# Performance work log

Hardware: AMD Instinct MI355X
Metric: run time of the kernel (lower is better)

Reference implementation:

```python
import jax, jax.numpy as jnp
import numpy as np


def _eta(pos, conj):
    # e[0] = pos[:,1::2] repeated into even/odd cols; e[1] = (+/-)pos[:,0::2] likewise
    c = jnp.repeat(pos[:, 1::2], 2, axis=1)
    s = jnp.repeat(pos[:, 0::2], 2, axis=1)
    return jnp.stack([c, s if conj else -s])  # [2, N, d]


def setup_inputs() -> dict:
    key = jax.random.key(0)
    ks = jax.random.split(key, 8)
    B, N, d, H = 8, 4096, 128, 4
    s = 0.02
    return {
        "x": jax.random.normal(ks[0], (B, N, d), jnp.float32),
        "pos": jax.random.normal(ks[1], (N, d), jnp.float32),
        "W_lt": jax.random.normal(ks[2], (d, d), jnp.float32) * s,
        "W_phi": jax.random.normal(ks[3], (d * H, d), jnp.float32) * s,
        "b_phi": jnp.zeros((d * H,), jnp.float32),
        "W_c1": jax.random.normal(ks[4], (H, H), jnp.float32) * s,
        "b_c1": jnp.zeros((H,), jnp.float32),
        "W_c2": jax.random.normal(ks[5], (1, H), jnp.float32) * s,
        "b_c2": jnp.zeros((1,), jnp.float32),
        "ln_g": jnp.ones((d,), jnp.float32),
        "ln_b": jnp.zeros((d,), jnp.float32),
        "W_f1": jax.random.normal(ks[6], (d, d), jnp.float32) * s,
        "b_f1": jnp.zeros((d,), jnp.float32),
        "W_f2": jax.random.normal(ks[7], (d, d), jnp.float32) * s,
        "b_f2": jnp.zeros((d,), jnp.float32),
    }


def reference(x, pos, W_lt, W_phi, b_phi, W_c1, b_c1, W_c2, b_c2,
              ln_g, ln_b, W_f1, b_f1, W_f2, b_f2):
    B, N, d = x.shape
    H = W_phi.shape[0] // d
    x = x @ W_lt.T                                   # linear_trans (no bias)
    e = _eta(pos, False)                             # [2,N,d]
    xe = x[None] * e[:, None]                        # [2,B,N,d]
    # A = ones(N,N) - I  =>  A @ v == sum over nodes minus self
    f = xe.sum(axis=2, keepdims=True) - xe           # [2,B,N,d]
    f_norm = jnp.sqrt(f[0] ** 2 + f[1] ** 2)         # [B,N,d]
    phi = ((x + pos[None]) @ W_phi.T + b_phi).reshape(B, N, H, d)
    # ReLU1(|f| - phi): relu(min(1, f_norm - phi))
    res = jax.nn.relu(jnp.minimum(1.0, f_norm[:, :, None, :] - phi))  # [B,N,H,d]
    ce = _eta(pos, True)
    fec = f[0] * ce[0][None] - f[1] * ce[1][None]    # [B,N,d]
    rfe = res * fec[:, :, None, :]                   # [B,N,H,d]
    # inverse transform: (1/N) * (M @ A) with A symmetric => sum-minus-self over node dim
    inv = (rfe.sum(axis=1, keepdims=True) - rfe) / N  # [B,N,H,d]
    t = inv.transpose(0, 1, 3, 2)                    # [B,N,d,H]
    comb = (jax.nn.relu(t @ W_c1.T + b_c1) @ W_c2.T + b_c2)[..., 0]  # [B,N,d]
    m = x + comb
    mu = m.mean(-1, keepdims=True)
    var = ((m - mu) ** 2).mean(-1, keepdims=True)
    mn = (m - mu) * jax.lax.rsqrt(var + 1e-6) * ln_g + ln_b
    return jax.nn.relu(mn @ W_f1.T + b_f1) @ W_f2.T + b_f2
```

## Files before the change

### kernel.cpp

```cpp
#include <hip/hip_runtime.h>
#include <hip/hip_bf16.h>


#define DEV __device__ __forceinline__

typedef __attribute__((ext_vector_type(8))) short bf16x8;
typedef __attribute__((ext_vector_type(4))) float f32x4;

constexpr int Bb = 8, Nn = 4096;
constexpr int BN = Bb * Nn;
constexpr int LDP = 136;
constexpr int P8  = 144;

union U8 { ushort u[8]; uint4 v; };

static DEV ushort f2bf(float f) {
    __hip_bfloat16 h = __float2bfloat16(f);
    return *reinterpret_cast<unsigned short*>(&h);
}
static DEV float bf2f(ushort u) {
    return __bfloat162float(*reinterpret_cast<const __hip_bfloat16*>(&u));
}
static DEV unsigned char f2fp8(float f) {
    return (unsigned char)(__builtin_amdgcn_cvt_pk_fp8_f32(f, f, 0u, false) & 0xff);
}

__global__ __launch_bounds__(256) void k_fused1(
    const float* __restrict__ X, const float* __restrict__ Wlt,
    const float* __restrict__ Wphi, const float* __restrict__ bphi,
    const float* __restrict__ pos, ushort* __restrict__ x1b,
    unsigned char* __restrict__ phi8, float* __restrict__ PS)
{
    __shared__ __align__(16) ushort xs[64 * LDP];
    __shared__ __align__(16) ushort wsl[128 * LDP];
    __shared__ __align__(16) unsigned char aux[64 * P8];
    float (*red)[2][128] = reinterpret_cast<float (*)[2][128]>(aux);
    unsigned char* p8 = aux;

    const int t = threadIdx.x;
    const int row0 = blockIdx.x * 64;
    const int w = t >> 6, l = t & 63;
    const int lr = l & 15;
    const int lk = (l >> 4) * 8;

    #pragma unroll
    for (int i = 0; i < 4; ++i) {
        int e = t + i * 256, r = e >> 4, c = (e & 15) * 8;
        const float* p = X + (size_t)(row0 + r) * 128 + c;
        float4 a = *reinterpret_cast<const float4*>(p);
        float4 b = *reinterpret_cast<const float4*>(p + 4);
        U8 u;
        u.u[0] = f2bf(a.x); u.u[1] = f2bf(a.y); u.u[2] = f2bf(a.z); u.u[3] = f2bf(a.w);
        u.u[4] = f2bf(b.x); u.u[5] = f2bf(b.y); u.u[6] = f2bf(b.z); u.u[7] = f2bf(b.w);
        *reinterpret_cast<uint4*>(xs + r * LDP + c) = u.v;
    }
    #pragma unroll
    for (int i = 0; i < 8; ++i) {
        int e = t + i * 256, r = e >> 4, c = (e & 15) * 8;
        const float* p = Wlt + (size_t)r * 128 + c;
        float4 a = *reinterpret_cast<const float4*>(p);
        float4 b = *reinterpret_cast<const float4*>(p + 4);
        U8 u;
        u.u[0] = f2bf(a.x); u.u[1] = f2bf(a.y); u.u[2] = f2bf(a.z); u.u[3] = f2bf(a.w);
        u.u[4] = f2bf(b.x); u.u[5] = f2bf(b.y); u.u[6] = f2bf(b.z); u.u[7] = f2bf(b.w);
        *reinterpret_cast<uint4*>(wsl + r * LDP + c) = u.v;
    }
    __syncthreads();

    {
        f32x4 acc[8];
        #pragma unroll
        for (int cf = 0; cf < 8; ++cf) acc[cf] = f32x4{0.f, 0.f, 0.f, 0.f};
        #pragma unroll
        for (int ks = 0; ks < 4; ++ks) {
            bf16x8 a = *reinterpret_cast<const bf16x8*>(xs + (w * 16 + lr) * LDP + ks * 32 + lk);
            #pragma unroll
            for (int cf = 0; cf < 8; ++cf) {
                bf16x8 b = *reinterpret_cast<const bf16x8*>(wsl + (cf * 16 + lr) * LDP + ks * 32 + lk);
                acc[cf] = __builtin_amdgcn_mfma_f32_16x16x32_bf16(a, b, acc[cf], 0, 0, 0);
            }
        }
        __syncthreads();

        #pragma unroll
        for (int cf = 0; cf < 8; ++cf) {
            int col = cf * 16 + lr;
            #pragma unroll
            for (int reg = 0; reg < 4; ++reg) {
                int rl = w * 16 + (l >> 4) * 4 + reg;
                xs[rl * LDP + col] = f2bf(acc[cf][reg]);
            }
        }
    }
    __syncthreads();

    #pragma unroll
    for (int i = 0; i < 4; ++i) {
        int e = t + i * 256, r = e >> 4, c = (e & 15) * 8;
        uint4 v = *reinterpret_cast<const uint4*>(xs + r * LDP + c);
        *reinterpret_cast<uint4*>(x1b + (size_t)(row0 + r) * 128 + c) = v;
    }
    {
        int c2 = t & 63, g = t >> 6;
        float a0e = 0.f, a1e = 0.f, a0o = 0.f, a1o = 0.f;
        #pragma unroll 4
        for (int i = 0; i < 16; ++i) {
            int r = g * 16 + i;
            int n = (row0 + r) & (Nn - 1);
            unsigned int v = *reinterpret_cast<const unsigned int*>(xs + r * LDP + 2 * c2);
            float lo = bf2f((ushort)(v & 0xffff));
            float hi = bf2f((ushort)(v >> 16));
            float2 p = *reinterpret_cast<const float2*>(pos + (size_t)n * 128 + 2 * c2);
            a0e += lo * p.y; a1e += lo * p.x;
            a0o += hi * p.y; a1o += hi * p.x;
        }
        red[g][0][2 * c2] = a0e; red[g][0][2 * c2 + 1] = a0o;
        red[g][1][2 * c2] = a1e; red[g][1][2 * c2 + 1] = a1o;
    }
    __syncthreads();

    {
        int half = t >> 7, col = t & 127;
        float s = red[0][half][col] + red[1][half][col] + red[2][half][col] + red[3][half][col];
        PS[(size_t)blockIdx.x * 256 + t] = s;
    }
    #pragma unroll
    for (int i = 0; i < 4; ++i) {
        int e = t + i * 256, r = e >> 4, c = (e & 15) * 8;
        U8 u;
        u.v = *reinterpret_cast<const uint4*>(xs + r * LDP + c);
        int n = (row0 + r) & (Nn - 1);
        const float* q = pos + (size_t)n * 128 + c;
        float4 pa = *reinterpret_cast<const float4*>(q);
        float4 pb = *reinterpret_cast<const float4*>(q + 4);
        u.u[0] = f2bf(bf2f(u.u[0]) + pa.x);
        u.u[1] = f2bf(bf2f(u.u[1]) + pa.y);
        u.u[2] = f2bf(bf2f(u.u[2]) + pa.z);
        u.u[3] = f2bf(bf2f(u.u[3]) + pa.w);
        u.u[4] = f2bf(bf2f(u.u[4]) + pb.x);
        u.u[5] = f2bf(bf2f(u.u[5]) + pb.y);
        u.u[6] = f2bf(bf2f(u.u[6]) + pb.z);
        u.u[7] = f2bf(bf2f(u.u[7]) + pb.w);
        *reinterpret_cast<uint4*>(xs + r * LDP + c) = u.v;
    }

    for (int jt = 0; jt < 4; ++jt) {
        __syncthreads();
        {
            const float* Wt = Wphi + (size_t)jt * 128 * 128;
            #pragma unroll
            for (int i = 0; i < 8; ++i) {
                int e = t + i * 256, r = e >> 4, c = (e & 15) * 8;
                const float* p = Wt + (size_t)r * 128 + c;
                float4 a = *reinterpret_cast<const float4*>(p);
                float4 b = *reinterpret_cast<const float4*>(p + 4);
                U8 u;
                u.u[0] = f2bf(a.x); u.u[1] = f2bf(a.y); u.u[2] = f2bf(a.z); u.u[3] = f2bf(a.w);
                u.u[4] = f2bf(b.x); u.u[5] = f2bf(b.y); u.u[6] = f2bf(b.z); u.u[7] = f2bf(b.w);
                *reinterpret_cast<uint4*>(wsl + r * LDP + c) = u.v;
            }
            if (jt > 0) {
                #pragma unroll
                for (int i = 0; i < 2; ++i) {
                    int e = t + i * 256, r = e >> 3, c = (e & 7) * 16;
                    uint4 v = *reinterpret_cast<const uint4*>(p8 + r * P8 + c);
                    *reinterpret_cast<uint4*>(phi8 + (size_t)(row0 + r) * 512 + (jt - 1) * 128 + c) = v;
                }
            }
        }
        __syncthreads();

        f32x4 acc[8];
        #pragma unroll
        for (int cf = 0; cf < 8; ++cf) acc[cf] = f32x4{0.f, 0.f, 0.f, 0.f};
        #pragma unroll
        for (int ks = 0; ks < 4; ++ks) {
            bf16x8 a = *reinterpret_cast<const bf16x8*>(xs + (w * 16 + lr) * LDP + ks * 32 + lk);
            #pragma unroll
            for (int cf = 0; cf < 8; ++cf) {
                bf16x8 b = *reinterpret_cast<const bf16x8*>(wsl + (cf * 16 + lr) * LDP + ks * 32 + lk);
                acc[cf] = __builtin_amdgcn_mfma_f32_16x16x32_bf16(a, b, acc[cf], 0, 0, 0);
            }
        }
        #pragma unroll
        for (int cf = 0; cf < 8; ++cf) {
            int col = cf * 16 + lr;
            float bv = bphi[jt * 128 + col];
            #pragma unroll
            for (int reg = 0; reg < 4; ++reg) {
                int rl = w * 16 + (l >> 4) * 4 + reg;
                p8[rl * P8 + col] = f2fp8(acc[cf][reg] + bv);
            }
        }
    }
    __syncthreads();
    #pragma unroll
    for (int i = 0; i < 2; ++i) {
        int e = t + i * 256, r = e >> 3, c = (e & 7) * 16;
        uint4 v = *reinterpret_cast<const uint4*>(p8 + r * P8 + c);
        *reinterpret_cast<uint4*>(phi8 + (size_t)(row0 + r) * 512 + 3 * 128 + c) = v;
    }
}

__global__ __launch_bounds__(256) void k_finS(
    const float* __restrict__ PS, float* __restrict__ S0, float* __restrict__ S1)
{
    int b = blockIdx.x, t = threadIdx.x;
    float s = 0.f;
    #pragma unroll 8
    for (int c = 0; c < 64; ++c) s += PS[(size_t)(b * 64 + c) * 256 + t];
    if (t < 128) S0[b * 128 + t] = s;
    else         S1[b * 128 + (t - 128)] = s;
}

__global__ __launch_bounds__(256) void k_reduceT(
    const ushort* __restrict__ x1b, const unsigned char* __restrict__ phi8,
    const float* __restrict__ pos, const float* __restrict__ S0,
    const float* __restrict__ S1, float* __restrict__ PT)
{
    int b = blockIdx.x >> 6, c64 = blockIdx.x & 63;
    int rr = threadIdx.x >> 5, d0 = (threadIdx.x & 31) * 4;
    float4 S0v = *reinterpret_cast<const float4*>(S0 + b * 128 + d0);
    float4 S1v = *reinterpret_cast<const float4*>(S1 + b * 128 + d0);
    float S0a[4] = {S0v.x, S0v.y, S0v.z, S0v.w};
    float S1a[4] = {S1v.x, S1v.y, S1v.z, S1v.w};
    float acc[4][4];
    #pragma unroll
    for (int h = 0; h < 4; ++h)
        #pragma unroll
        for (int j = 0; j < 4; ++j) acc[h][j] = 0.f;

    #pragma unroll 2
    for (int i = 0; i < 8; ++i) {
        int n = c64 * 64 + i * 8 + rr;
        size_t r = (size_t)b * Nn + n;
        ushort4 xv4 = *reinterpret_cast<const ushort4*>(x1b + r * 128 + d0);
        float4 p = *reinterpret_cast<const float4*>(pos + (size_t)n * 128 + d0);
        float xv[4] = {bf2f(xv4.x), bf2f(xv4.y), bf2f(xv4.z), bf2f(xv4.w)};
        float cc[4] = {p.y, p.y, p.w, p.w};
        float ss[4] = {p.x, p.x, p.z, p.z};
        float fec[4], fn[4];
        #pragma unroll
        for (int j = 0; j < 4; ++j) {
            float f0 = S0a[j] - xv[j] * cc[j];
            float f1 = xv[j] * ss[j] - S1a[j];
            fn[j] = sqrtf(f0 * f0 + f1 * f1);
            fec[j] = f0 * cc[j] - f1 * ss[j];
        }
        #pragma unroll
        for (int h = 0; h < 4; ++h) {
            unsigned int pv = *reinterpret_cast<const unsigned int*>(phi8 + r * 512 + h * 128 + d0);
            float ph0 = __builtin_amdgcn_cvt_f32_fp8(pv, 0);
            float ph1 = __builtin_amdgcn_cvt_f32_fp8(pv, 1);
            float ph2 = __builtin_amdgcn_cvt_f32_fp8(pv, 2);
            float ph3 = __builtin_amdgcn_cvt_f32_fp8(pv, 3);
            acc[h][0] += fmaxf(0.f, fminf(1.f, fn[0] - ph0)) * fec[0];
            acc[h][1] += fmaxf(0.f, fminf(1.f, fn[1] - ph1)) * fec[1];
            acc[h][2] += fmaxf(0.f, fminf(1.f, fn[2] - ph2)) * fec[2];
            acc[h][3] += fmaxf(0.f, fminf(1.f, fn[3] - ph3)) * fec[3];
        }
    }
    __shared__ float red[8][512];
    #pragma unroll
    for (int h = 0; h < 4; ++h)
        #pragma unroll
        for (int j = 0; j < 4; ++j) red[rr][h * 128 + d0 + j] = acc[h][j];
    __syncthreads();
    int tt = threadIdx.x;
    #pragma unroll
    for (int q = 0; q < 2; ++q) {
        int idx = tt + q * 256;
        float s = 0.f;
        #pragma unroll
        for (int k = 0; k < 8; ++k) s += red[k][idx];
        PT[(size_t)blockIdx.x * 512 + idx] = s;
    }
}

__global__ __launch_bounds__(256) void k_finT(
    const float* __restrict__ PT, float* __restrict__ T)
{
    int idx = blockIdx.x * 256 + threadIdx.x;
    int b = idx >> 9, lo = idx & 511;
    float s = 0.f;
    #pragma unroll 8
    for (int c = 0; c < 64; ++c) s += PT[(size_t)b * 32768 + c * 512 + lo];
    T[idx] = s;
}

__global__ __launch_bounds__(256) void k_comb_ffn(
    const ushort* __restrict__ x1b, const unsigned char* __restrict__ phi8,
    const float* __restrict__ pos, const float* __restrict__ S0,
    const float* __restrict__ S1, const float* __restrict__ T,
    const float* __restrict__ Wc1, const float* __restrict__ bc1,
    const float* __restrict__ Wc2, const float* __restrict__ bc2,
    const float* __restrict__ lng, const float* __restrict__ lnb,
    const float* __restrict__ Wf1, const float* __restrict__ bf1,
    const float* __restrict__ Wf2, const float* __restrict__ bf2,
    float* __restrict__ out)
{
    __shared__ __align__(16) ushort xs[64 * LDP];
    __shared__ __align__(16) ushort wsl[128 * LDP];
    const int t = threadIdx.x;
    const int row0 = blockIdx.x * 64;
    const int w = t >> 6, l = t & 63;

    #pragma unroll
    for (int i = 0; i < 8; ++i) {
        int e = t + i * 256, r = e >> 4, c = (e & 15) * 8;
        const float* p = Wf1 + (size_t)r * 128 + c;
        float4 a = *reinterpret_cast<const float4*>(p);
        float4 b = *reinterpret_cast<const float4*>(p + 4);
        U8 u;
        u.u[0] = f2bf(a.x); u.u[1] = f2bf(a.y); u.u[2] = f2bf(a.z); u.u[3] = f2bf(a.w);
        u.u[4] = f2bf(b.x); u.u[5] = f2bf(b.y); u.u[6] = f2bf(b.z); u.u[7] = f2bf(b.w);
        *reinterpret_cast<uint4*>(wsl + r * LDP + c) = u.v;
    }

    {
        const int d0 = 2 * l;
        const float g0 = lng[d0], g1 = lng[d0 + 1];
        const float be0 = lnb[d0], be1 = lnb[d0 + 1];
        const float c2v[4] = {Wc2[0], Wc2[1], Wc2[2], Wc2[3]};
        const float b2v = bc2[0];
        for (int i = 0; i < 16; ++i) {
            int rl = w * 16 + i;
            int rrow = row0 + rl;
            int b = rrow >> 12;
            int n = rrow & 4095;
            size_t r = (size_t)rrow;

            ushort2 xv2 = *reinterpret_cast<const ushort2*>(x1b + r * 128 + d0);
            float2 p2 = *reinterpret_cast<const float2*>(pos + (size_t)n * 128 + d0);
            float2 s0 = *reinterpret_cast<const float2*>(S0 + b * 128 + d0);
            float2 s1 = *reinterpret_cast<const float2*>(S1 + b * 128 + d0);
            float cc = p2.y, ss = p2.x;
            float xv[2] = {bf2f(xv2.x), bf2f(xv2.y)};
            float S0a[2] = {s0.x, s0.y}, S1a[2] = {s1.x, s1.y};
            float2 Tv[4];
            #pragma unroll
            for (int h = 0; h < 4; ++h)
                Tv[h] = *reinterpret_cast<const float2*>(T + (b * 4 + h) * 128 + d0);
            float phv[4][2];
            #pragma unroll
            for (int h = 0; h < 4; ++h) {
                unsigned int pu = *reinterpret_cast<const ushort*>(phi8 + r * 512 + h * 128 + d0);
                phv[h][0] = __builtin_amdgcn_cvt_f32_fp8(pu, 0);
                phv[h][1] = __builtin_amdgcn_cvt_f32_fp8(pu, 1);
            }

            float m[2];
            #pragma unroll
            for (int q = 0; q < 2; ++q) {
                float f0 = S0a[q] - xv[q] * cc;
                float f1 = xv[q] * ss - S1a[q];
                float fn = sqrtf(f0 * f0 + f1 * f1);
                float fec = f0 * cc - f1 * ss;
                float inv[4];
                #pragma unroll
                for (int h = 0; h < 4; ++h) {
                    float res = fmaxf(0.f, fminf(1.f, fn - phv[h][q]));
                    float tv = q ? Tv[h].y : Tv[h].x;
                    inv[h] = (tv - res * fec) * (1.f / (float)Nn);
                }
                float comb = b2v;
                #pragma unroll
                for (int h = 0; h < 4; ++h) {
                    float u = bc1[h];
                    #pragma unroll
                    for (int h2 = 0; h2 < 4; ++h2) u += Wc1[h * 4 + h2] * inv[h2];
                    comb += fmaxf(u, 0.f) * c2v[h];
                }
                m[q] = xv[q] + comb;
            }

            float s = m[0] + m[1];
            #pragma unroll
            for (int off = 32; off; off >>= 1) s += __shfl_xor(s, off);
            float mu = s * (1.f / 128.f);
            float e0 = m[0] - mu, e1 = m[1] - mu;
            float v = e0 * e0 + e1 * e1;
            #pragma unroll
            for (int off = 32; off; off >>= 1) v += __shfl_xor(v, off);
            float rstd = rsqrtf(v * (1.f / 128.f) + 1e-6f);
            ushort2 o;
            o.x = f2bf(e0 * rstd * g0 + be0);
            o.y = f2bf(e1 * rstd * g1 + be1);
            *reinterpret_cast<ushort2*>(xs + rl * LDP + d0) = o;
        }
    }
    __syncthreads();

    const int lr = l & 15;
    const int lk = (l >> 4) * 8;

    f32x4 acc[8];
    #pragma unroll
    for (int cf = 0; cf < 8; ++cf) acc[cf] = f32x4{0.f, 0.f, 0.f, 0.f};
    #pragma unroll
    for (int ks = 0; ks < 4; ++ks) {
        bf16x8 a = *reinterpret_cast<const bf16x8*>(xs + (w * 16 + lr) * LDP + ks * 32 + lk);
        #pragma unroll
        for (int cf = 0; cf < 8; ++cf) {
            bf16x8 b = *reinterpret_cast<const bf16x8*>(wsl + (cf * 16 + lr) * LDP + ks * 32 + lk);
            acc[cf] = __builtin_amdgcn_mfma_f32_16x16x32_bf16(a, b, acc[cf], 0, 0, 0);
        }
    }
    __syncthreads();

    #pragma unroll
    for (int cf = 0; cf < 8; ++cf) {
        int col = cf * 16 + lr;
        float bv = bf1[col];
        #pragma unroll
        for (int reg = 0; reg < 4; ++reg) {
            int rl = w * 16 + (l >> 4) * 4 + reg;
            xs[rl * LDP + col] = f2bf(fmaxf(acc[cf][reg] + bv, 0.f));
        }
    }
    #pragma unroll
    for (int i = 0; i < 8; ++i) {
        int e = t + i * 256, r = e >> 4, c = (e & 15) * 8;
        const float* p = Wf2 + (size_t)r * 128 + c;
        float4 a = *reinterpret_cast<const float4*>(p);
        float4 b = *reinterpret_cast<const float4*>(p + 4);
        U8 u;
        u.u[0] = f2bf(a.x); u.u[1] = f2bf(a.y); u.u[2] = f2bf(a.z); u.u[3] = f2bf(a.w);
        u.u[4] = f2bf(b.x); u.u[5] = f2bf(b.y); u.u[6] = f2bf(b.z); u.u[7] = f2bf(b.w);
        *reinterpret_cast<uint4*>(wsl + r * LDP + c) = u.v;
    }
    __syncthreads();

    #pragma unroll
    for (int cf = 0; cf < 8; ++cf) acc[cf] = f32x4{0.f, 0.f, 0.f, 0.f};
    #pragma unroll
    for (int ks = 0; ks < 4; ++ks) {
        bf16x8 a = *reinterpret_cast<const bf16x8*>(xs + (w * 16 + lr) * LDP + ks * 32 + lk);
        #pragma unroll
        for (int cf = 0; cf < 8; ++cf) {
            bf16x8 b = *reinterpret_cast<const bf16x8*>(wsl + (cf * 16 + lr) * LDP + ks * 32 + lk);
            acc[cf] = __builtin_amdgcn_mfma_f32_16x16x32_bf16(a, b, acc[cf], 0, 0, 0);
        }
    }
    #pragma unroll
    for (int cf = 0; cf < 8; ++cf) {
        int col = cf * 16 + lr;
        float bv = bf2[col];
        #pragma unroll
        for (int reg = 0; reg < 4; ++reg) {
            int r = row0 + w * 16 + (l >> 4) * 4 + reg;
            out[(size_t)r * 128 + col] = acc[cf][reg] + bv;
        }
    }
}

extern "C" void kernel_launch(void* const* d_in, const int* in_sizes, int n_in,
                              void* d_out, int out_size, void* d_ws, size_t ws_size,
                              hipStream_t stream)
{
    const float* x    = (const float*)d_in[0];
    const float* pos  = (const float*)d_in[1];
    const float* Wlt  = (const float*)d_in[2];
    const float* Wphi = (const float*)d_in[3];
    const float* bphi = (const float*)d_in[4];
    const float* Wc1  = (const float*)d_in[5];
    const float* bc1  = (const float*)d_in[6];
    const float* Wc2  = (const float*)d_in[7];
    const float* bc2  = (const float*)d_in[8];
    const float* lng  = (const float*)d_in[9];
    const float* lnb  = (const float*)d_in[10];
    const float* Wf1  = (const float*)d_in[11];
    const float* bf1  = (const float*)d_in[12];
    const float* Wf2  = (const float*)d_in[13];
    const float* bf2  = (const float*)d_in[14];

    float* ws = (float*)d_ws;
    ushort* x1b = (ushort*)ws;
    float* S0   = ws + 2097152;
    float* S1   = S0 + 1024;
    float* T    = S1 + 1024;
    float* PS   = T + 4096;
    float* PT   = PS + 131072;
    unsigned char* phi8 = (unsigned char*)(ws + 2496512);
    float* out  = (float*)d_out;

    k_fused1<<<dim3(BN / 64), 256, 0, stream>>>(x, Wlt, Wphi, bphi, pos, x1b, phi8, PS);
    k_finS<<<dim3(Bb), 256, 0, stream>>>(PS, S0, S1);
    k_reduceT<<<dim3(512), 256, 0, stream>>>(x1b, phi8, pos, S0, S1, PT);
    k_finT<<<dim3(16), 256, 0, stream>>>(PT, T);
    k_comb_ffn<<<dim3(BN / 64), 256, 0, stream>>>(x1b, phi8, pos, S0, S1, T,
                                                  Wc1, bc1, Wc2, bc2, lng, lnb,
                                                  Wf1, bf1, Wf2, bf2, out);
}
```

Baseline: 70.43 us.

## Pre-convert weights to bf16 once and merge reductions into cooperative kernel

Adds a prep kernel that converts all weight matrices to bf16 in workspace, so the 512 blocks of each GEMM kernel no longer repeat the fp32 load and bf16 conversion. It also replaces the three small reduction kernels (finS, reduceT, finT) with one cooperative kernel that uses grid-wide syncs between phases and warp-shuffle reductions. The aim is to cut launch overhead and redundant conversion work. The cost is one extra launch and a dependency on cooperative launch, which needs all 512 blocks resident at once, plus grid-sync overhead.

```diff
diff --git a/kernel.cpp b/kernel.cpp
--- a/kernel.cpp
+++ b/kernel.cpp
@@ -1,5 +1,8 @@
 #include <hip/hip_runtime.h>
 #include <hip/hip_bf16.h>
+#include <hip/hip_cooperative_groups.h>
+
+namespace cg = cooperative_groups;
 
 
 #define DEV __device__ __forceinline__
@@ -25,9 +28,30 @@
     return (unsigned char)(__builtin_amdgcn_cvt_pk_fp8_f32(f, f, 0u, false) & 0xff);
 }
 
+__global__ __launch_bounds__(256) void k_prep(
+    const float* __restrict__ Wlt, const float* __restrict__ Wphi,
+    const float* __restrict__ Wf1, const float* __restrict__ Wf2,
+    ushort* __restrict__ wbLt, ushort* __restrict__ wbPhi,
+    ushort* __restrict__ wbF1, ushort* __restrict__ wbF2)
+{
+    int bx = blockIdx.x;
+    const float* src; ushort* dst; int off;
+    if (bx < 8)       { src = Wlt;  dst = wbLt;  off = bx * 2048; }
+    else if (bx < 40) { src = Wphi; dst = wbPhi; off = (bx - 8) * 2048; }
+    else if (bx < 48) { src = Wf1;  dst = wbF1;  off = (bx - 40) * 2048; }
+    else              { src = Wf2;  dst = wbF2;  off = (bx - 48) * 2048; }
+    int e = off + threadIdx.x * 8;
+    float4 a = *reinterpret_cast<const float4*>(src + e);
+    float4 b = *reinterpret_cast<const float4*>(src + e + 4);
+    U8 u;
+    u.u[0] = f2bf(a.x); u.u[1] = f2bf(a.y); u.u[2] = f2bf(a.z); u.u[3] = f2bf(a.w);
+    u.u[4] = f2bf(b.x); u.u[5] = f2bf(b.y); u.u[6] = f2bf(b.z); u.u[7] = f2bf(b.w);
+    *reinterpret_cast<uint4*>(dst + e) = u.v;
+}
+
 __global__ __launch_bounds__(256) void k_fused1(
-    const float* __restrict__ X, const float* __restrict__ Wlt,
-    const float* __restrict__ Wphi, const float* __restrict__ bphi,
+    const float* __restrict__ X, const ushort* __restrict__ wbLt,
+    const ushort* __restrict__ wbPhi, const float* __restrict__ bphi,
     const float* __restrict__ pos, ushort* __restrict__ x1b,
     unsigned char* __restrict__ phi8, float* __restrict__ PS)
 {
@@ -57,13 +81,8 @@
     #pragma unroll
     for (int i = 0; i < 8; ++i) {
         int e = t + i * 256, r = e >> 4, c = (e & 15) * 8;
-        const float* p = Wlt + (size_t)r * 128 + c;
-        float4 a = *reinterpret_cast<const float4*>(p);
-        float4 b = *reinterpret_cast<const float4*>(p + 4);
-        U8 u;
-        u.u[0] = f2bf(a.x); u.u[1] = f2bf(a.y); u.u[2] = f2bf(a.z); u.u[3] = f2bf(a.w);
-        u.u[4] = f2bf(b.x); u.u[5] = f2bf(b.y); u.u[6] = f2bf(b.z); u.u[7] = f2bf(b.w);
-        *reinterpret_cast<uint4*>(wsl + r * LDP + c) = u.v;
+        uint4 v = *reinterpret_cast<const uint4*>(wbLt + (size_t)r * 128 + c);
+        *reinterpret_cast<uint4*>(wsl + r * LDP + c) = v;
     }
     __syncthreads();
 
@@ -147,17 +166,12 @@
     for (int jt = 0; jt < 4; ++jt) {
         __syncthreads();
         {
-            const float* Wt = Wphi + (size_t)jt * 128 * 128;
+            const ushort* Wt = wbPhi + (size_t)jt * 128 * 128;
             #pragma unroll
             for (int i = 0; i < 8; ++i) {
                 int e = t + i * 256, r = e >> 4, c = (e & 15) * 8;
-                const float* p = Wt + (size_t)r * 128 + c;
-                float4 a = *reinterpret_cast<const float4*>(p);
-                float4 b = *reinterpret_cast<const float4*>(p + 4);
-                U8 u;
-                u.u[0] = f2bf(a.x); u.u[1] = f2bf(a.y); u.u[2] = f2bf(a.z); u.u[3] = f2bf(a.w);
-                u.u[4] = f2bf(b.x); u.u[5] = f2bf(b.y); u.u[6] = f2bf(b.z); u.u[7] = f2bf(b.w);
-                *reinterpret_cast<uint4*>(wsl + r * LDP + c) = u.v;
+                uint4 v = *reinterpret_cast<const uint4*>(Wt + (size_t)r * 128 + c);
+                *reinterpret_cast<uint4*>(wsl + r * LDP + c) = v;
             }
             if (jt > 0) {
                 #pragma unroll
@@ -202,90 +216,101 @@
     }
 }
 
-__global__ __launch_bounds__(256) void k_finS(
-    const float* __restrict__ PS, float* __restrict__ S0, float* __restrict__ S1)
+__global__ __launch_bounds__(256) void k_coop_ST(
+    const ushort* __restrict__ x1b, const unsigned char* __restrict__ phi8,
+    const float* __restrict__ pos, const float* __restrict__ PS,
+    float* __restrict__ S0, float* __restrict__ S1,
+    float* __restrict__ PT, float* __restrict__ T)
 {
-    int b = blockIdx.x, t = threadIdx.x;
-    float s = 0.f;
-    #pragma unroll 8
-    for (int c = 0; c < 64; ++c) s += PS[(size_t)(b * 64 + c) * 256 + t];
-    if (t < 128) S0[b * 128 + t] = s;
-    else         S1[b * 128 + (t - 128)] = s;
-}
-
-__global__ __launch_bounds__(256) void k_reduceT(
-    const ushort* __restrict__ x1b, const unsigned char* __restrict__ phi8,
-    const float* __restrict__ pos, const float* __restrict__ S0,
-    const float* __restrict__ S1, float* __restrict__ PT)
-{
-    int b = blockIdx.x >> 6, c64 = blockIdx.x & 63;
-    int rr = threadIdx.x >> 5, d0 = (threadIdx.x & 31) * 4;
-    float4 S0v = *reinterpret_cast<const float4*>(S0 + b * 128 + d0);
-    float4 S1v = *reinterpret_cast<const float4*>(S1 + b * 128 + d0);
-    float S0a[4] = {S0v.x, S0v.y, S0v.z, S0v.w};
-    float S1a[4] = {S1v.x, S1v.y, S1v.z, S1v.w};
-    float acc[4][4];
-    #pragma unroll
-    for (int h = 0; h < 4; ++h)
-        #pragma unroll
-        for (int j = 0; j < 4; ++j) acc[h][j] = 0.f;
-
-    #pragma unroll 2
-    for (int i = 0; i < 8; ++i) {
-        int n = c64 * 64 + i * 8 + rr;
-        size_t r = (size_t)b * Nn + n;
-        ushort4 xv4 = *reinterpret_cast<const ushort4*>(x1b + r * 128 + d0);
-        float4 p = *reinterpret_cast<const float4*>(pos + (size_t)n * 128 + d0);
-        float xv[4] = {bf2f(xv4.x), bf2f(xv4.y), bf2f(xv4.z), bf2f(xv4.w)};
-        float cc[4] = {p.y, p.y, p.w, p.w};
-        float ss[4] = {p.x, p.x, p.z, p.z};
-        float fec[4], fn[4];
-        #pragma unroll
-        for (int j = 0; j < 4; ++j) {
-            float f0 = S0a[j] - xv[j] * cc[j];
-            float f1 = xv[j] * ss[j] - S1a[j];
-            fn[j] = sqrtf(f0 * f0 + f1 * f1);
-            fec[j] = f0 * cc[j] - f1 * ss[j];
-        }
-        #pragma unroll
-        for (int h = 0; h < 4; ++h) {
-            unsigned int pv = *reinterpret_cast<const unsigned int*>(phi8 + r * 512 + h * 128 + d0);
-            float ph0 = __builtin_amdgcn_cvt_f32_fp8(pv, 0);
-            float ph1 = __builtin_amdgcn_cvt_f32_fp8(pv, 1);
-            float ph2 = __builtin_amdgcn_cvt_f32_fp8(pv, 2);
-            float ph3 = __builtin_amdgcn_cvt_f32_fp8(pv, 3);
-            acc[h][0] += fmaxf(0.f, fminf(1.f, fn[0] - ph0)) * fec[0];
-            acc[h][1] += fmaxf(0.f, fminf(1.f, fn[1] - ph1)) * fec[1];
-            acc[h][2] += fmaxf(0.f, fminf(1.f, fn[2] - ph2)) * fec[2];
-            acc[h][3] += fmaxf(0.f, fminf(1.f, fn[3] - ph3)) * fec[3];
-        }
-    }
-    __shared__ float red[8][512];
-    #pragma unroll
-    for (int h = 0; h < 4; ++h)
-        #pragma unroll
-        for (int j = 0; j < 4; ++j) red[rr][h * 128 + d0 + j] = acc[h][j];
-    __syncthreads();
-    int tt = threadIdx.x;
-    #pragma unroll
-    for (int q = 0; q < 2; ++q) {
-        int idx = tt + q * 256;
-        float s = 0.f;
-        #pragma unroll
-        for (int k = 0; k < 8; ++k) s += red[k][idx];
-        PT[(size_t)blockIdx.x * 512 + idx] = s;
-    }
-}
-
-__global__ __launch_bounds__(256) void k_finT(
-    const float* __restrict__ PT, float* __restrict__ T)
-{
-    int idx = blockIdx.x * 256 + threadIdx.x;
-    int b = idx >> 9, lo = idx & 511;
-    float s = 0.f;
-    #pragma unroll 8
-    for (int c = 0; c < 64; ++c) s += PT[(size_t)b * 32768 + c * 512 + lo];
-    T[idx] = s;
+    cg::grid_group grid = cg::this_grid();
+
+    {
+        int idx = blockIdx.x * 4 + (threadIdx.x >> 6);
+        int lane = threadIdx.x & 63;
+        int b = idx >> 8, tcol = idx & 255;
+        float s = PS[(size_t)(b * 64 + lane) * 256 + tcol];
+        #pragma unroll
+        for (int off = 32; off; off >>= 1) s += __shfl_xor(s, off);
+        if (lane == 0) {
+            if (tcol < 128) S0[b * 128 + tcol] = s;
+            else            S1[b * 128 + (tcol - 128)] = s;
+        }
+    }
+    __threadfence();
+    grid.sync();
+
+    {
+        int b = blockIdx.x >> 6, c64 = blockIdx.x & 63;
+        int rr = threadIdx.x >> 5, d0 = (threadIdx.x & 31) * 4;
+        float4 S0v = *reinterpret_cast<const float4*>(S0 + b * 128 + d0);
+        float4 S1v = *reinterpret_cast<const float4*>(S1 + b * 128 + d0);
+        float S0a[4] = {S0v.x, S0v.y, S0v.z, S0v.w};
+        float S1a[4] = {S1v.x, S1v.y, S1v.z, S1v.w};
+        float acc[4][4];
+        #pragma unroll
+        for (int h = 0; h < 4; ++h)
+            #pragma unroll
+            for (int j = 0; j < 4; ++j) acc[h][j] = 0.f;
+
+        #pragma unroll 2
+        for (int i = 0; i < 8; ++i) {
+            int n = c64 * 64 + i * 8 + rr;
+            size_t r = (size_t)b * Nn + n;
+            ushort4 xv4 = *reinterpret_cast<const ushort4*>(x1b + r * 128 + d0);
+            float4 p = *reinterpret_cast<const float4*>(pos + (size_t)n * 128 + d0);
+            float xv[4] = {bf2f(xv4.x), bf2f(xv4.y), bf2f(xv4.z), bf2f(xv4.w)};
+            float cc[4] = {p.y, p.y, p.w, p.w};
+            float ss[4] = {p.x, p.x, p.z, p.z};
+            float fec[4], fn[4];
+            #pragma unroll
+            for (int j = 0; j < 4; ++j) {
+                float f0 = S0a[j] - xv[j] * cc[j];
+                float f1 = xv[j] * ss[j] - S1a[j];
+                fn[j] = sqrtf(f0 * f0 + f1 * f1);
+                fec[j] = f0 * cc[j] - f1 * ss[j];
+            }
+            #pragma unroll
+            for (int h = 0; h < 4; ++h) {
+                unsigned int pv = *reinterpret_cast<const unsigned int*>(phi8 + r * 512 + h * 128 + d0);
+                float ph0 = __builtin_amdgcn_cvt_f32_fp8(pv, 0);
+                float ph1 = __builtin_amdgcn_cvt_f32_fp8(pv, 1);
+                float ph2 = __builtin_amdgcn_cvt_f32_fp8(pv, 2);
+                float ph3 = __builtin_amdgcn_cvt_f32_fp8(pv, 3);
+                acc[h][0] += fmaxf(0.f, fminf(1.f, fn[0] - ph0)) * fec[0];
+                acc[h][1] += fmaxf(0.f, fminf(1.f, fn[1] - ph1)) * fec[1];
+                acc[h][2] += fmaxf(0.f, fminf(1.f, fn[2] - ph2)) * fec[2];
+                acc[h][3] += fmaxf(0.f, fminf(1.f, fn[3] - ph3)) * fec[3];
+            }
+        }
+        __shared__ float red[8][512];
+        #pragma unroll
+        for (int h = 0; h < 4; ++h)
+            #pragma unroll
+            for (int j = 0; j < 4; ++j) red[rr][h * 128 + d0 + j] = acc[h][j];
+        __syncthreads();
+        int tt = threadIdx.x;
+        #pragma unroll
+        for (int q = 0; q < 2; ++q) {
+            int idx = tt + q * 256;
+            float s = 0.f;
+            #pragma unroll
+            for (int k = 0; k < 8; ++k) s += red[k][idx];
+            PT[(size_t)blockIdx.x * 512 + idx] = s;
+        }
+    }
+    __threadfence();
+    grid.sync();
+
+    {
+        int o = threadIdx.x >> 5, ll = threadIdx.x & 31;
+        int idx = blockIdx.x * 8 + o;
+        int b = idx >> 9, lo = idx & 511;
+        float s = PT[(size_t)b * 32768 + ll * 512 + lo]
+                + PT[(size_t)b * 32768 + (ll + 32) * 512 + lo];
+        #pragma unroll
+        for (int off = 16; off; off >>= 1) s += __shfl_xor(s, off);
+        if (ll == 0) T[idx] = s;
+    }
 }
 
 __global__ __launch_bounds__(256) void k_comb_ffn(
@@ -295,8 +320,8 @@
     const float* __restrict__ Wc1, const float* __restrict__ bc1,
     const float* __restrict__ Wc2, const float* __restrict__ bc2,
     const float* __restrict__ lng, const float* __restrict__ lnb,
-    const float* __restrict__ Wf1, const float* __restrict__ bf1,
-    const float* __restrict__ Wf2, const float* __restrict__ bf2,
+    const ushort* __restrict__ wbF1, const float* __restrict__ bf1,
+    const ushort* __restrict__ wbF2, const float* __restrict__ bf2,
     float* __restrict__ out)
 {
     __shared__ __align__(16) ushort xs[64 * LDP];
@@ -308,13 +333,8 @@
     #pragma unroll
     for (int i = 0; i < 8; ++i) {
         int e = t + i * 256, r = e >> 4, c = (e & 15) * 8;
-        const float* p = Wf1 + (size_t)r * 128 + c;
-        float4 a = *reinterpret_cast<const float4*>(p);
-        float4 b = *reinterpret_cast<const float4*>(p + 4);
-        U8 u;
-        u.u[0] = f2bf(a.x); u.u[1] = f2bf(a.y); u.u[2] = f2bf(a.z); u.u[3] = f2bf(a.w);
-        u.u[4] = f2bf(b.x); u.u[5] = f2bf(b.y); u.u[6] = f2bf(b.z); u.u[7] = f2bf(b.w);
-        *reinterpret_cast<uint4*>(wsl + r * LDP + c) = u.v;
+        uint4 v = *reinterpret_cast<const uint4*>(wbF1 + (size_t)r * 128 + c);
+        *reinterpret_cast<uint4*>(wsl + r * LDP + c) = v;
     }
 
     {
@@ -421,13 +441,8 @@
     #pragma unroll
     for (int i = 0; i < 8; ++i) {
         int e = t + i * 256, r = e >> 4, c = (e & 15) * 8;
-        const float* p = Wf2 + (size_t)r * 128 + c;
-        float4 a = *reinterpret_cast<const float4*>(p);
-        float4 b = *reinterpret_cast<const float4*>(p + 4);
-        U8 u;
-        u.u[0] = f2bf(a.x); u.u[1] = f2bf(a.y); u.u[2] = f2bf(a.z); u.u[3] = f2bf(a.w);
-        u.u[4] = f2bf(b.x); u.u[5] = f2bf(b.y); u.u[6] = f2bf(b.z); u.u[7] = f2bf(b.w);
-        *reinterpret_cast<uint4*>(wsl + r * LDP + c) = u.v;
+        uint4 v = *reinterpret_cast<const uint4*>(wbF2 + (size_t)r * 128 + c);
+        *reinterpret_cast<uint4*>(wsl + r * LDP + c) = v;
     }
     __syncthreads();
 
@@ -482,13 +497,22 @@
     float* PS   = T + 4096;
     float* PT   = PS + 131072;
     unsigned char* phi8 = (unsigned char*)(ws + 2496512);
+    ushort* wbLt  = (ushort*)(ws + 6690816);
+    ushort* wbPhi = wbLt + 16384;
+    ushort* wbF1  = wbPhi + 65536;
+    ushort* wbF2  = wbF1 + 16384;
     float* out  = (float*)d_out;
 
-    k_fused1<<<dim3(BN / 64), 256, 0, stream>>>(x, Wlt, Wphi, bphi, pos, x1b, phi8, PS);
-    k_finS<<<dim3(Bb), 256, 0, stream>>>(PS, S0, S1);
-    k_reduceT<<<dim3(512), 256, 0, stream>>>(x1b, phi8, pos, S0, S1, PT);
-    k_finT<<<dim3(16), 256, 0, stream>>>(PT, T);
+    k_prep<<<dim3(56), 256, 0, stream>>>(Wlt, Wphi, Wf1, Wf2, wbLt, wbPhi, wbF1, wbF2);
+    k_fused1<<<dim3(BN / 64), 256, 0, stream>>>(x, wbLt, wbPhi, bphi, pos, x1b, phi8, PS);
+    {
+        const ushort* a0 = x1b; const unsigned char* a1 = phi8; const float* a2 = pos;
+        const float* a3 = PS; float* a4 = S0; float* a5 = S1; float* a6 = PT; float* a7 = T;
+        void* args[] = {&a0, &a1, &a2, &a3, &a4, &a5, &a6, &a7};
+        hipLaunchCooperativeKernel((const void*)k_coop_ST, dim3(512), dim3(256),
+                                   args, 0, stream);
+    }
     k_comb_ffn<<<dim3(BN / 64), 256, 0, stream>>>(x1b, phi8, pos, S0, S1, T,
                                                   Wc1, bc1, Wc2, bc2, lng, lnb,
-                                                  Wf1, bf1, Wf2, bf2, out);
-}
+                                                  wbF1, bf1, wbF2, bf2, out);
+}
```

Measured after the change: 233.7 us. 3.32x slower.
